# Kernel optimization log

Hardware: AMD Instinct MI355X
Metric: run time of the kernel (lower is better)

Reference implementation:

```python
import jax, jax.numpy as jnp
import numpy as np

DIM = 512
HEADS = 8
DIM_HEAD = 64
INNER = HEADS * DIM_HEAD          # 512
CPB_DIM = DIM // 2                # 256 (ContinuousPositionBias hidden dim)
FF_INNER = int(DIM * 4 * 2 / 3)   # 1365 (GEGLU inner dim)
B, C, F, H, W = 2, 512, 8, 32, 32
SCALE = DIM_HEAD ** -0.5


def setup_inputs() -> dict:
    key = jax.random.key(0)
    ks = jax.random.split(key, 24)
    def rnd(k, shape, s=0.02):
        return jax.random.normal(k, shape, jnp.float32) * s
    return {
        "x": jax.random.normal(ks[0], (B, C, F, W, W), jnp.float32)[:, :, :, :H, :],
        # spatial attention
        "sa_gamma": jnp.ones((DIM,), jnp.float32),
        "sa_wq": rnd(ks[1], (DIM, INNER)),
        "sa_wkv": rnd(ks[2], (DIM, 2 * INNER)),
        "sa_wo": rnd(ks[3], (INNER, DIM)),
        # temporal attention
        "ta_gamma": jnp.ones((DIM,), jnp.float32),
        "ta_wq": rnd(ks[4], (DIM, INNER)),
        "ta_wkv": rnd(ks[5], (DIM, 2 * INNER)),
        "ta_wo": rnd(ks[6], (INNER, DIM)),
        # spatial ContinuousPositionBias MLP (num_dims=2, layers=2)
        "sp_w1": rnd(ks[7], (2, CPB_DIM), 0.1), "sp_b1": jnp.zeros((CPB_DIM,), jnp.float32),
        "sp_w2": rnd(ks[8], (CPB_DIM, CPB_DIM), 0.05), "sp_b2": jnp.zeros((CPB_DIM,), jnp.float32),
        "sp_w3": rnd(ks[9], (CPB_DIM, HEADS), 0.05), "sp_b3": jnp.zeros((HEADS,), jnp.float32),
        # temporal ContinuousPositionBias MLP (num_dims=1)
        "tp_w1": rnd(ks[10], (1, CPB_DIM), 0.1), "tp_b1": jnp.zeros((CPB_DIM,), jnp.float32),
        "tp_w2": rnd(ks[11], (CPB_DIM, CPB_DIM), 0.05), "tp_b2": jnp.zeros((CPB_DIM,), jnp.float32),
        "tp_w3": rnd(ks[12], (CPB_DIM, HEADS), 0.05), "tp_b3": jnp.zeros((HEADS,), jnp.float32),
        # FeedForward: Conv3d 1x1 (no bias) -> GEGLU -> RMSNorm -> Conv3d 1x1
        "ff_win": rnd(ks[13], (DIM, 2 * FF_INNER)),
        "ff_gamma": jnp.ones((FF_INNER,), jnp.float32),
        "ff_wout": rnd(ks[14], (FF_INNER, DIM)),
    }


def _rms_last(x, g):
    # torch: F.normalize(x, dim=-1) * sqrt(C) * gamma
    nrm = jnp.sqrt(jnp.sum(x * x, axis=-1, keepdims=True))
    return x / jnp.maximum(nrm, 1e-12) * jnp.sqrt(jnp.float32(x.shape[-1])) * g


def _mlp_bias(rel, w1, b1, w2, b2, w3, b3):
    h = jax.nn.silu(rel @ w1 + b1)
    h = jax.nn.silu(h @ w2 + b2)
    return h @ w3 + b3  # [R, heads]


def _cpb_2d(h, w, params):
    ry = jnp.arange(-(h - 1), h, dtype=jnp.float32)
    rx = jnp.arange(-(w - 1), w, dtype=jnp.float32)
    gy, gx = jnp.meshgrid(ry, rx, indexing='ij')
    rel = jnp.stack([gy, gx], -1).reshape(-1, 2)          # [(2h-1)(2w-1), 2]
    tab = _mlp_bias(rel, *params)                          # [R, heads]
    py, px = jnp.meshgrid(jnp.arange(h), jnp.arange(w), indexing='ij')
    pos = jnp.stack([py.reshape(-1), px.reshape(-1)], -1)  # [n, 2]
    d = pos[:, None, :] - pos[None, :, :]                  # [n, n, 2]
    idx = (d[..., 0] + h - 1) * (2 * w - 1) + (d[..., 1] + w - 1)
    return jnp.transpose(tab[idx], (2, 0, 1))              # [heads, n, n]


def _cpb_1d(f, params):
    rel = jnp.arange(-(f - 1), f, dtype=jnp.float32)[:, None]
    tab = _mlp_bias(rel, *params)                          # [2f-1, heads]
    p = jnp.arange(f)
    idx = p[:, None] - p[None, :] + f - 1
    return jnp.transpose(tab[idx], (2, 0, 1))              # [heads, f, f]


def _attn(x, gamma, wq, wkv, wo, bias):
    # x: [b, n, c]; manual softmax(QK^T*scale + bias)V (flash disabled by pos_bias)
    xn = _rms_last(x, gamma)
    q = xn @ wq
    k, v = jnp.split(xn @ wkv, 2, axis=-1)
    b, n, _ = q.shape
    rs = lambda t: t.reshape(b, n, HEADS, DIM_HEAD).transpose(0, 2, 1, 3)
    q, k, v = rs(q), rs(k), rs(v)
    s = jnp.einsum('bhid,bhjd->bhij', q, k) * SCALE + bias[None]
    a = jax.nn.softmax(s, axis=-1)
    o = jnp.einsum('bhij,bhjd->bhid', a, v)
    o = o.transpose(0, 2, 1, 3).reshape(b, n, INNER)
    return o @ wo


def _ff(x, win, gamma, wout):
    # x: [b, f, h, w, c] channel-last; Conv3d 1x1 == channel einsum
    hdn = jnp.einsum('bfhwc,co->bfhwo', x, win)
    a, gate = jnp.split(hdn, 2, axis=-1)
    y = a * jax.nn.gelu(gate, approximate=False)           # GEGLU (torch exact gelu)
    # shift_token: chunk channels, shift second half by +1 frame
    c1 = (FF_INNER + 1) // 2
    t1, t2 = y[..., :c1], y[..., c1:]
    t2 = jnp.pad(t2, ((0, 0), (1, 0), (0, 0), (0, 0), (0, 0)))[:, :-1]
    y = jnp.concatenate([t1, t2], axis=-1)
    yn = _rms_last(y, gamma)                               # RMSNorm over channels
    return jnp.einsum('bfhwi,ic->bfhwc', yn, wout)


def reference(x, sa_gamma, sa_wq, sa_wkv, sa_wo, ta_gamma, ta_wq, ta_wkv, ta_wo,
              sp_w1, sp_b1, sp_w2, sp_b2, sp_w3, sp_b3,
              tp_w1, tp_b1, tp_w2, tp_b2, tp_w3, tp_b3,
              ff_win, ff_gamma, ff_wout):
    b, c, f, h, w = x.shape
    xl = jnp.transpose(x, (0, 2, 3, 4, 1))                 # b f h w c
    # spatial attention over (h w) tokens, batched over (b f)
    xs = xl.reshape(b * f, h * w, c)
    sp_bias = _cpb_2d(h, w, (sp_w1, sp_b1, sp_w2, sp_b2, sp_w3, sp_b3))
    xs = _attn(xs, sa_gamma, sa_wq, sa_wkv, sa_wo, sp_bias) + xs
    xv = xs.reshape(b, f, h, w, c)
    # temporal attention over f tokens, batched over (b h w)
    xt = jnp.transpose(xv, (0, 2, 3, 1, 4)).reshape(b * h * w, f, c)
    tp_bias = _cpb_1d(f, (tp_w1, tp_b1, tp_w2, tp_b2, tp_w3, tp_b3))
    xt = _attn(xt, ta_gamma, ta_wq, ta_wkv, ta_wo, tp_bias) + xt
    xv = jnp.transpose(xt.reshape(b, h, w, f, c), (0, 3, 1, 2, 4))
    # GEGLU feedforward with token shift
    xv = _ff(xv, ff_win, ff_gamma, ff_wout) + xv
    return jnp.transpose(xv, (0, 4, 1, 2, 3))              # b c f h w
```

## Files before the change

kernel.cpp:

```cpp
#include <hip/hip_runtime.h>
#include <cstdint>
#include <cstddef>

typedef __bf16 bf16_t;
typedef __bf16 bf16x8 __attribute__((ext_vector_type(8)));
typedef __bf16 bf16x4 __attribute__((ext_vector_type(4)));
typedef float floatx4 __attribute__((ext_vector_type(4)));

__device__ __forceinline__ float wred_sum(float v) {
#pragma unroll
  for (int off = 32; off > 0; off >>= 1) v += __shfl_xor(v, off);
  return v;
}
__device__ __forceinline__ void async16(const void* g, void* l) {
  __builtin_amdgcn_global_load_lds((const __attribute__((address_space(1))) void*)g,
                                   (__attribute__((address_space(3))) void*)l, 16, 0, 0);
}

template <int MODE>
__global__ __launch_bounds__(256) void st_gemm(
    const bf16_t* __restrict__ A, const bf16_t* __restrict__ B, void* Cp, void* Cp2,
    const float* Res, int M, int N, int K, int lda, int ldb, int ldc) {
  __shared__ bf16_t sA[3][128 * 32];
  __shared__ bf16_t sB[3][128 * 32];
  const int tid = threadIdx.x;
  const int bm = blockIdx.x, bn = blockIdx.y;
  const int lane = tid & 63;
  const int wave = tid >> 6;
  const int wm = (wave >> 1) * 64, wn = (wave & 1) * 64;
  const int rowf = lane & 15, qc = lane >> 4;
  const int fco = (qc ^ ((rowf >> 1) & 3)) * 8;

  const bf16_t* aSrc[2];
  const bf16_t* bSrc[2];
  int sOff[2];
#pragma unroll
  for (int it = 0; it < 2; ++it) {
    int slot = it * 256 + tid;
    int mi = slot >> 2, kc = slot & 3;
    int cs = kc ^ ((mi >> 1) & 3);
    int ar = bm * 128 + mi; if (ar > M - 1) ar = M - 1;
    int br = bn * 128 + mi; if (br > N - 1) br = N - 1;
    aSrc[it] = A + (size_t)ar * lda + cs * 8;
    bSrc[it] = B + (size_t)br * ldb + cs * 8;
    sOff[it] = slot * 16;
  }

  floatx4 acc[4][4];
#pragma unroll
  for (int i = 0; i < 4; ++i)
#pragma unroll
    for (int j = 0; j < 4; ++j) acc[i][j] = floatx4{0.f, 0.f, 0.f, 0.f};

  const int NT = K >> 5;
#pragma unroll
  for (int it = 0; it < 2; ++it) {
    async16(aSrc[it], (char*)sA[0] + sOff[it]);
    async16(bSrc[it], (char*)sB[0] + sOff[it]);
  }
#pragma unroll
  for (int it = 0; it < 2; ++it) {
    async16(aSrc[it] + 32, (char*)sA[1] + sOff[it]);
    async16(bSrc[it] + 32, (char*)sB[1] + sOff[it]);
  }
  __builtin_amdgcn_sched_barrier(0);
  asm volatile("s_waitcnt vmcnt(4)" ::: "memory");
  __builtin_amdgcn_s_barrier();
  __builtin_amdgcn_sched_barrier(0);

  int bcur = 0, bnx = 2;
#pragma unroll 1
  for (int t = 0; t < NT; ++t) {
    const bf16_t* sAc = sA[bcur];
    const bf16_t* sBc = sB[bcur];
    bf16x8 af[4], bv[4];
#pragma unroll
    for (int i = 0; i < 4; ++i) {
      af[i] = *(const bf16x8*)(sAc + (wm + i * 16 + rowf) * 32 + fco);
      bv[i] = *(const bf16x8*)(sBc + (wn + i * 16 + rowf) * 32 + fco);
    }
    if (t + 2 < NT) {
      const int kt2 = (t + 2) * 32;
#pragma unroll
      for (int it = 0; it < 2; ++it) {
        async16(aSrc[it] + kt2, (char*)sA[bnx] + sOff[it]);
        async16(bSrc[it] + kt2, (char*)sB[bnx] + sOff[it]);
      }
    }
#pragma unroll
    for (int i = 0; i < 4; ++i)
#pragma unroll
      for (int j = 0; j < 4; ++j)
        acc[i][j] = __builtin_amdgcn_mfma_f32_16x16x32_bf16(af[i], bv[j], acc[i][j], 0, 0, 0);
    if (t + 1 < NT) {
      __builtin_amdgcn_sched_barrier(0);
      if (t + 2 < NT) asm volatile("s_waitcnt vmcnt(4)" ::: "memory");
      else            asm volatile("s_waitcnt vmcnt(0)" ::: "memory");
      __builtin_amdgcn_s_barrier();
      __builtin_amdgcn_sched_barrier(0);
    }
    bcur = (bcur == 2) ? 0 : bcur + 1;
    bnx = (bnx == 2) ? 0 : bnx + 1;
  }

  const int cl = lane & 15;
  const int rowBase = bm * 128 + wm + (lane >> 4) * 4;
  if (MODE == 5) {
    bf16_t* yb = (bf16_t*)Cp;
    const int cg0 = ((bn * 128 + wn) >> 5) * 16;
#pragma unroll
    for (int i = 0; i < 4; ++i) {
#pragma unroll
      for (int p = 0; p < 2; ++p) {
        int c = cg0 + p * 16 + cl;
        if (c >= 1365) continue;
#pragma unroll
        for (int r = 0; r < 4; ++r) {
          int row = rowBase + i * 16 + r;
          if (row >= M) continue;
          float a = acc[i][2 * p][r];
          float gt = acc[i][2 * p + 1][r];
          float zz = gt * (0.7978845608f + 0.03567740814f * gt * gt);
          float u = __builtin_exp2f(-2.8853900817779268f * zz);
          float y = a * gt / (1.f + u);
          yb[(size_t)row * ldc + c] = (bf16_t)y;
        }
      }
    }
    return;
  }
  const int colBase = bn * 128 + wn + cl;
#pragma unroll
  for (int i = 0; i < 4; ++i) {
#pragma unroll
    for (int j = 0; j < 4; ++j) {
      int col = colBase + j * 16;
      if (col >= N) continue;
#pragma unroll
      for (int r = 0; r < 4; ++r) {
        int row = rowBase + i * 16 + r;
        if (row >= M) continue;
        long long inidx = (long long)row * ldc + col;
        float v = acc[i][j][r];
        if (MODE >= 2) v += Res[inidx];
        if (MODE == 1) { ((bf16_t*)Cp)[inidx] = (bf16_t)v; }
        else if (MODE == 2) { ((float*)Cp)[inidx] = v; }
        else if (MODE == 3) {
          int orow = (row & ~8191) | ((row & 1023) << 3) | ((row >> 10) & 7);
          ((float*)Cp)[(long long)orow * ldc + col] = v;
        } else if (MODE == 4) {
          int orow = (row & ~8191) | ((row & 7) << 10) | ((row >> 3) & 1023);
          long long oidx = (long long)orow * ldc + col;
          ((float*)Cp)[oidx] = v;
          ((bf16_t*)Cp2)[oidx] = (bf16_t)v;
        }
      }
    }
  }
}

__global__ __launch_bounds__(256) void st_transpose2d(
    const float* __restrict__ in, float* __restrict__ out, int R, int Cc,
    long long inb, long long outb) {
  __shared__ float tile[32][33];
  const int ct = blockIdx.x, rt = blockIdx.y, b = blockIdx.z;
  in += (long long)b * inb;
  out += (long long)b * outb;
  const int tx = threadIdx.x & 31, ty = threadIdx.x >> 5;
#pragma unroll
  for (int k = 0; k < 4; ++k) {
    int r = rt * 32 + ty + k * 8;
    int c = ct * 32 + tx;
    tile[ty + k * 8][tx] = in[(size_t)r * Cc + c];
  }
  __syncthreads();
#pragma unroll
  for (int k = 0; k < 4; ++k) {
    int c = ct * 32 + ty + k * 8;
    int r = rt * 32 + tx;
    out[(size_t)c * R + r] = tile[tx][ty + k * 8];
  }
}

__global__ void st_wtrans(const float* __restrict__ src, bf16_t* __restrict__ dst,
                          int K, int Kpad, int N, int srcld, int coloff, long total) {
  long idx = (long)blockIdx.x * 256 + threadIdx.x;
  if (idx >= total) return;
  int kp = (int)(idx % Kpad);
  int n = (int)(idx / Kpad);
  float v = (kp < K) ? src[(size_t)kp * srcld + coloff + n] : 0.f;
  dst[idx] = (bf16_t)v;
}

__global__ void st_wtrans_geglu(const float* __restrict__ src, bf16_t* __restrict__ dst,
                                long total) {
  long idx = (long)blockIdx.x * 256 + threadIdx.x;
  if (idx >= total) return;
  int kp = (int)(idx & 511);
  int n = (int)(idx >> 9);
  int c = ((n >> 5) << 4) + (n & 15);
  float v = 0.f;
  if (c < 1365) {
    int srccol = c + (((n >> 4) & 1) ? 1365 : 0);
    v = src[(size_t)kp * 2730 + srccol];
  }
  dst[idx] = (bf16_t)v;
}

__global__ __launch_bounds__(256) void st_cpb(
    const float* __restrict__ w1, const float* __restrict__ b1,
    const float* __restrict__ w2, const float* __restrict__ b2,
    const float* __restrict__ w3, const float* __restrict__ b3,
    float* __restrict__ tab2d, float* __restrict__ tab1d, int two_d) {
  const int pos = blockIdx.x, t = threadIdx.x;
  float r0, r1 = 0.f;
  if (two_d) { r0 = (float)(pos / 63 - 31); r1 = (float)(pos % 63 - 31); }
  else { r0 = (float)(pos - 7); }
  __shared__ float sh[256];
  float h = r0 * w1[t] + (two_d ? r1 * w1[256 + t] : 0.f) + b1[t];
  h = h / (1.f + expf(-h));
  sh[t] = h;
  __syncthreads();
  float h2 = b2[t];
  for (int j = 0; j < 256; ++j) h2 += sh[j] * w2[j * 256 + t];
  h2 = h2 / (1.f + expf(-h2));
  __syncthreads();
  sh[t] = h2;
  __syncthreads();
  if (t < 8) {
    float o = b3[t];
    for (int j = 0; j < 256; ++j) o += sh[j] * w3[j * 8 + t];
    if (two_d) tab2d[t * 4000 + pos] = o * 8.0f;
    else tab1d[t * 15 + pos] = o;
  }
}

__global__ __launch_bounds__(256) void st_rmsnorm(const float* __restrict__ x,
                                                  const float* __restrict__ gamma,
                                                  bf16_t* __restrict__ y) {
  const int token = blockIdx.x * 4 + (threadIdx.x >> 6);
  const int lane = threadIdx.x & 63;
  const float* xr = x + (size_t)token * 512;
  float v[8];
  float ss = 0.f;
#pragma unroll
  for (int k = 0; k < 8; ++k) { v[k] = xr[k * 64 + lane]; ss += v[k] * v[k]; }
  ss = wred_sum(ss);
  const float r = 22.627416998f / fmaxf(sqrtf(ss), 1e-12f);
  bf16_t* yr = y + (size_t)token * 512;
#pragma unroll
  for (int k = 0; k < 8; ++k) yr[k * 64 + lane] = (bf16_t)(v[k] * r * gamma[k * 64 + lane]);
}

__global__ __launch_bounds__(256) void st_vtrans(const bf16_t* __restrict__ qkv,
                                                 bf16_t* __restrict__ vT) {
  __shared__ float tile[32][33];
  const int jt = blockIdx.x, dt = blockIdx.y, z = blockIdx.z;
  const int bf = z >> 3, h = z & 7;
  const int tx = threadIdx.x & 31, ty = threadIdx.x >> 5;
#pragma unroll
  for (int k = 0; k < 4; ++k) {
    int j = jt * 32 + ty + k * 8;
    int d = dt * 32 + tx;
    tile[ty + k * 8][tx] = (float)qkv[((size_t)(bf * 1024 + j)) * 1536 + 1024 + h * 64 + d];
  }
  __syncthreads();
#pragma unroll
  for (int k = 0; k < 4; ++k) {
    int d = dt * 32 + ty + k * 8;
    int j = jt * 32 + tx;
    vT[((size_t)z * 64 + d) * 1024 + j] = (bf16_t)tile[tx][ty + k * 8];
  }
}

__global__ __launch_bounds__(256, 4) void st_flash(
    const bf16_t* __restrict__ qkv, const bf16_t* __restrict__ vT,
    const float* __restrict__ tab2f, bf16_t* __restrict__ ob) {
  __shared__ __align__(16) bf16_t ldsK[2][32 * 64];
  __shared__ __align__(16) bf16_t ldsV[2][64 * 32];
  __shared__ __align__(16) bf16_t ldsP[4 * 32 * 32];
  __shared__ __align__(16) float ldsT[2208];
  const int qtile = blockIdx.x;
  const int z = blockIdx.y;
  const int bf = z >> 3, h = z & 7;
  const int tid = threadIdx.x;
  const int lane = tid & 63, wave = tid >> 6;
  const int cl = lane & 15, g = lane >> 4;
  const size_t qkvBase = (size_t)bf * 1024 * 1536 + h * 64;
  const int eoff = (qtile * 252) & ~3;
  const bf16_t* Kp = qkv + qkvBase + 512;
  const bf16_t* Vp = vT + (size_t)z * 65536;

#pragma unroll
  for (int it = 0; it < 3; ++it) {
    int s = it * 256 + tid;
    if (s < 552) async16(tab2f + h * 4000 + eoff + s * 4, (char*)ldsT + s * 16);
  }
  {
    int row = tid >> 3, c = tid & 7, cs = c ^ (row & 7);
    async16(Kp + (size_t)row * 1536 + cs * 8, (char*)ldsK[0] + tid * 16);
    int rv = tid >> 2, cv = tid & 3, csv = cv ^ (rv & 3);
    async16(Vp + (size_t)rv * 1024 + csv * 8, (char*)ldsV[0] + tid * 16);
  }
  bf16x8 aq[2][2];
#pragma unroll
  for (int it = 0; it < 2; ++it)
#pragma unroll
    for (int ks = 0; ks < 2; ++ks) {
      int row = qtile * 128 + wave * 32 + it * 16 + cl;
      aq[it][ks] = *(const bf16x8*)(qkv + qkvBase + (size_t)row * 1536 + (ks * 4 + g) * 8);
    }
  __syncthreads();

  int fiB[2];
#pragma unroll
  for (int it = 0; it < 2; ++it) {
    int i = qtile * 128 + wave * 32 + it * 16 + cl;
    fiB[it] = (i >> 5) * 63 + (i & 31) + 1984 - eoff;
  }
  float lsum[2] = {0.f, 0.f};
  floatx4 oacc[4][2];
#pragma unroll
  for (int dt = 0; dt < 4; ++dt)
#pragma unroll
    for (int it = 0; it < 2; ++it) oacc[dt][it] = floatx4{0.f, 0.f, 0.f, 0.f};

  bf16_t* ldsPw = ldsP + wave * (32 * 32);
  const float SC = 0.18033688011112042f;

#pragma unroll 2
  for (int t = 0; t < 32; ++t) {
    const int p = t & 1;
    if (t < 31) {
      const int j1 = (t + 1) * 32;
      int row = tid >> 3, c = tid & 7, cs = c ^ (row & 7);
      async16(Kp + (size_t)(j1 + row) * 1536 + cs * 8, (char*)ldsK[p ^ 1] + tid * 16);
      int rv = tid >> 2, cv = tid & 3, csv = cv ^ (rv & 3);
      async16(Vp + (size_t)rv * 1024 + j1 + csv * 8, (char*)ldsV[p ^ 1] + tid * 16);
    }
    const int j0 = t * 32;
#pragma unroll
    for (int jt = 0; jt < 2; ++jt) {
      int jb = j0 + jt * 16 + g * 4;
      int fjb = (jb >> 5) * 63 + (jb & 31);
      floatx4 sj[2];
#pragma unroll
      for (int it = 0; it < 2; ++it) {
        int idx0 = fiB[it] - fjb;
        sj[it] = floatx4{ldsT[idx0], ldsT[idx0 - 1], ldsT[idx0 - 2], ldsT[idx0 - 3]};
      }
#pragma unroll
      for (int ks = 0; ks < 2; ++ks) {
        int row = jt * 16 + cl;
        bf16x8 kf = *(const bf16x8*)(ldsK[p] + row * 64 + (((ks * 4 + g) ^ (row & 7))) * 8);
#pragma unroll
        for (int it = 0; it < 2; ++it)
          sj[it] = __builtin_amdgcn_mfma_f32_16x16x32_bf16(kf, aq[it][ks], sj[it], 0, 0, 0);
      }
      int gg = jt * 2 + (g >> 1);
#pragma unroll
      for (int it = 0; it < 2; ++it) {
        float e0 = __builtin_exp2f(sj[it][0] * SC);
        float e1 = __builtin_exp2f(sj[it][1] * SC);
        float e2 = __builtin_exp2f(sj[it][2] * SC);
        float e3 = __builtin_exp2f(sj[it][3] * SC);
        lsum[it] += (e0 + e1) + (e2 + e3);
        bf16x4 pv = {(bf16_t)e0, (bf16_t)e1, (bf16_t)e2, (bf16_t)e3};
        *(bf16x4*)((char*)ldsPw + (it * 16 + cl) * 64 +
                   ((gg ^ (cl & 3)) * 16 + (g & 1) * 8)) = pv;
      }
    }
    {
      bf16x8 pB[2];
#pragma unroll
      for (int it = 0; it < 2; ++it)
        pB[it] = *(const bf16x8*)((char*)ldsPw + (it * 16 + cl) * 64 + ((g ^ (cl & 3)) * 16));
#pragma unroll
      for (int dt = 0; dt < 4; ++dt) {
        int row = dt * 16 + cl;
        bf16x8 vf = *(const bf16x8*)(ldsV[p] + row * 32 + ((g ^ (row & 3)) * 8));
#pragma unroll
        for (int it = 0; it < 2; ++it)
          oacc[dt][it] = __builtin_amdgcn_mfma_f32_16x16x32_bf16(vf, pB[it], oacc[dt][it], 0, 0, 0);
      }
    }
    __syncthreads();
  }
  float inv[2];
#pragma unroll
  for (int it = 0; it < 2; ++it) {
    float s = lsum[it];
    s += __shfl_xor(s, 16);
    s += __shfl_xor(s, 32);
    inv[it] = 1.f / s;
  }
#pragma unroll
  for (int it = 0; it < 2; ++it) {
    int i = qtile * 128 + wave * 32 + it * 16 + cl;
    size_t base = ((size_t)bf * 1024 + i) * 512 + h * 64 + g * 4;
#pragma unroll
    for (int dt = 0; dt < 4; ++dt) {
      bf16x4 ov = {(bf16_t)(oacc[dt][it][0] * inv[it]), (bf16_t)(oacc[dt][it][1] * inv[it]),
                   (bf16_t)(oacc[dt][it][2] * inv[it]), (bf16_t)(oacc[dt][it][3] * inv[it])};
      *(bf16x4*)(ob + base + dt * 16) = ov;
    }
  }
}

__global__ __launch_bounds__(256) void st_tattn2(const bf16_t* __restrict__ qkv,
                                                 const float* __restrict__ tabf,
                                                 bf16_t* __restrict__ o) {
  const int wg = blockIdx.x * 4 + (threadIdx.x >> 6);
  const int bhw = wg >> 3, head = wg & 7;
  const int lane = threadIdx.x & 63;
  const size_t base = (size_t)bhw * 8 * 1536 + head * 64 + lane;
  float q[8], k[8], v[8];
#pragma unroll
  for (int f = 0; f < 8; ++f) {
    q[f] = (float)qkv[base + (size_t)f * 1536];
    k[f] = (float)qkv[base + (size_t)f * 1536 + 512];
    v[f] = (float)qkv[base + (size_t)f * 1536 + 1024];
  }
  float p[64];
#pragma unroll
  for (int i = 0; i < 8; ++i)
#pragma unroll
    for (int j = 0; j < 8; ++j) p[i * 8 + j] = q[i] * k[j];
#pragma unroll
  for (int st = 32; st >= 1; st >>= 1) {
    const bool hi = (lane & st) != 0;
#pragma unroll
    for (int m = 0; m < st; ++m) {
      float give = hi ? p[m] : p[m + st];
      float keep = hi ? p[m + st] : p[m];
      p[m] = keep + __shfl_xor(give, st);
    }
  }
  const int i = lane >> 3, j = lane & 7;
  float e = __expf(p[0] * 0.125f + tabf[head * 15 + i - j + 7]);
  float sm = e;
  sm += __shfl_xor(sm, 1);
  sm += __shfl_xor(sm, 2);
  sm += __shfl_xor(sm, 4);
  const float prob = e / sm;
  float acc[8];
#pragma unroll
  for (int ii = 0; ii < 8; ++ii) acc[ii] = 0.f;
#pragma unroll
  for (int ii = 0; ii < 8; ++ii)
#pragma unroll
    for (int jj = 0; jj < 8; ++jj)
      acc[ii] += __shfl(prob, ii * 8 + jj) * v[jj];
#pragma unroll
  for (int ii = 0; ii < 8; ++ii)
    o[(size_t)(bhw * 8 + ii) * 512 + head * 64 + lane] = (bf16_t)acc[ii];
}

__global__ __launch_bounds__(256) void st_glu(const bf16_t* __restrict__ y,
                                              const float* __restrict__ gamma,
                                              bf16_t* __restrict__ yn) {
  const int t = blockIdx.x;
  const int tid = threadIdx.x;
  const int f = (t >> 10) & 7;
  float yv[6];
  float ss = 0.f;
#pragma unroll
  for (int kk = 0; kk < 6; ++kk) {
    int c = kk * 256 + tid;
    float v = 0.f;
    if (c < 1365) {
      long src = t;
      bool valid = true;
      if (c >= 683) { if (f == 0) valid = false; else src = t - 1024; }
      if (valid) v = (float)y[src * 1365 + c];
    }
    yv[kk] = v;
    ss += v * v;
  }
  __shared__ float red[4];
  ss = wred_sum(ss);
  if ((tid & 63) == 0) red[tid >> 6] = ss;
  __syncthreads();
  ss = red[0] + red[1] + red[2] + red[3];
  const float r = sqrtf(1365.f) / fmaxf(sqrtf(ss), 1e-12f);
#pragma unroll
  for (int kk = 0; kk < 6; ++kk) {
    int c = kk * 256 + tid;
    if (c < 1365) yn[(size_t)t * 1376 + c] = (bf16_t)(yv[kk] * r * gamma[c]);
  }
  if (tid < 11) yn[(size_t)t * 1376 + 1365 + tid] = (bf16_t)0.f;
}

extern "C" void kernel_launch(void* const* d_in, const int* in_sizes, int n_in,
                              void* d_out, int out_size, void* d_ws, size_t ws_size,
                              hipStream_t stream) {
  const float* x        = (const float*)d_in[0];
  const float* sa_gamma = (const float*)d_in[1];
  const float* sa_wq    = (const float*)d_in[2];
  const float* sa_wkv   = (const float*)d_in[3];
  const float* sa_wo    = (const float*)d_in[4];
  const float* ta_gamma = (const float*)d_in[5];
  const float* ta_wq    = (const float*)d_in[6];
  const float* ta_wkv   = (const float*)d_in[7];
  const float* ta_wo    = (const float*)d_in[8];
  const float* sp_w1 = (const float*)d_in[9];
  const float* sp_b1 = (const float*)d_in[10];
  const float* sp_w2 = (const float*)d_in[11];
  const float* sp_b2 = (const float*)d_in[12];
  const float* sp_w3 = (const float*)d_in[13];
  const float* sp_b3 = (const float*)d_in[14];
  const float* tp_w1 = (const float*)d_in[15];
  const float* tp_b1 = (const float*)d_in[16];
  const float* tp_w2 = (const float*)d_in[17];
  const float* tp_b2 = (const float*)d_in[18];
  const float* tp_w3 = (const float*)d_in[19];
  const float* tp_b3 = (const float*)d_in[20];
  const float* ff_win   = (const float*)d_in[21];
  const float* ff_gamma = (const float*)d_in[22];
  const float* ff_wout  = (const float*)d_in[23];
  float* outp = (float*)d_out;

  char* ws = (char*)d_ws;
  size_t off = 0;
  auto alloc = [&](size_t bytes) -> char* {
    char* p = ws + off;
    off += (bytes + 255) & ~(size_t)255;
    return p;
  };
  const long T = 16384;
  float*  xs  = (float*)alloc((size_t)T * 512 * 4);
  bf16_t* xn  = (bf16_t*)alloc((size_t)T * 512 * 2);
  char*   R2  = alloc((size_t)T * 1536 * 2);
  char*   R3  = alloc((size_t)T * 1536 * 2);
  char*   R4  = alloc((size_t)T * 1376 * 2);
  bf16_t* wqkvT_sa = (bf16_t*)alloc(1536ULL * 512 * 2);
  bf16_t* woT_sa   = (bf16_t*)alloc(512ULL * 512 * 2);
  bf16_t* wqkvT_ta = (bf16_t*)alloc(1536ULL * 512 * 2);
  bf16_t* woT_ta   = (bf16_t*)alloc(512ULL * 512 * 2);
  bf16_t* winT  = (bf16_t*)alloc(2752ULL * 512 * 2);
  bf16_t* woutT = (bf16_t*)alloc(512ULL * 1376 * 2);
  float*  tab2f = (float*)alloc(8 * 4000 * 4);
  float*  tabf  = (float*)alloc(8 * 15 * 4);

  bf16_t* qkv  = (bf16_t*)R2;
  bf16_t* ybuf = (bf16_t*)R2;
  bf16_t* vT   = (bf16_t*)R3;
  float*  xt   = (float*)R3;
  bf16_t* ob_s = xn;
  bf16_t* ob_t = (bf16_t*)R4;
  bf16_t* ynb  = (bf16_t*)R4;

  st_transpose2d<<<dim3(256, 16, 2), 256, 0, stream>>>(x, xs, 512, 8192,
                                                       (long long)512 * 8192, (long long)512 * 8192);
  auto wt = [&](const float* src, bf16_t* dst, int K, int Kpad, int N, int srcld, int coloff) {
    long tot = (long)N * Kpad;
    st_wtrans<<<dim3((tot + 255) / 256), 256, 0, stream>>>(src, dst, K, Kpad, N, srcld, coloff, tot);
  };
  wt(sa_wq, wqkvT_sa, 512, 512, 512, 512, 0);
  wt(sa_wkv, wqkvT_sa + 512 * 512, 512, 512, 1024, 1024, 0);
  wt(sa_wo, woT_sa, 512, 512, 512, 512, 0);
  wt(ta_wq, wqkvT_ta, 512, 512, 512, 512, 0);
  wt(ta_wkv, wqkvT_ta + 512 * 512, 512, 512, 1024, 1024, 0);
  wt(ta_wo, woT_ta, 512, 512, 512, 512, 0);
  st_wtrans_geglu<<<dim3((2752 * 512) / 256), 256, 0, stream>>>(ff_win, winT, 2752L * 512);
  wt(ff_wout, woutT, 1365, 1376, 512, 512, 0);
  st_cpb<<<dim3(3969), 256, 0, stream>>>(sp_w1, sp_b1, sp_w2, sp_b2, sp_w3, sp_b3, tab2f, tabf, 1);
  st_cpb<<<dim3(15), 256, 0, stream>>>(tp_w1, tp_b1, tp_w2, tp_b2, tp_w3, tp_b3, tab2f, tabf, 0);

  st_rmsnorm<<<dim3(4096), 256, 0, stream>>>(xs, sa_gamma, xn);
  st_gemm<1><<<dim3(128, 12), 256, 0, stream>>>(
      xn, wqkvT_sa, (void*)qkv, nullptr, nullptr, 16384, 1536, 512, 512, 512, 1536);
  st_vtrans<<<dim3(32, 2, 128), 256, 0, stream>>>(qkv, vT);
  st_flash<<<dim3(8, 128), 256, 0, stream>>>(qkv, vT, tab2f, ob_s);
  st_gemm<3><<<dim3(128, 4), 256, 0, stream>>>(
      ob_s, woT_sa, (void*)xt, nullptr, xs, 16384, 512, 512, 512, 512, 512);

  st_rmsnorm<<<dim3(4096), 256, 0, stream>>>(xt, ta_gamma, xn);
  st_gemm<1><<<dim3(128, 12), 256, 0, stream>>>(
      xn, wqkvT_ta, (void*)qkv, nullptr, nullptr, 16384, 1536, 512, 512, 512, 1536);
  st_tattn2<<<dim3(4096), 256, 0, stream>>>(qkv, tabf, ob_t);
  st_gemm<4><<<dim3(128, 4), 256, 0, stream>>>(
      ob_t, woT_ta, (void*)xs, (void*)xn, xt, 16384, 512, 512, 512, 512, 512);

  st_gemm<5><<<dim3(128, 22), 256, 0, stream>>>(
      xn, winT, (void*)ybuf, nullptr, nullptr, 16384, 2752, 512, 512, 512, 1365);
  st_glu<<<dim3(16384), 256, 0, stream>>>(ybuf, ff_gamma, ynb);
  st_gemm<2><<<dim3(128, 4), 256, 0, stream>>>(
      ynb, woutT, (void*)xs, nullptr, xs, 16384, 512, 1376, 1376, 1376, 512);

  st_transpose2d<<<dim3(16, 256, 2), 256, 0, stream>>>(xs, outp, 8192, 512,
                                                       (long long)8192 * 512, (long long)8192 * 512);
}
```

Baseline: 654.9 us.

## Triple-buffer K in flash attention, read V directly from global, swap grid order

The spatial flash-attention kernel now keeps K in a three-stage LDS ring with prefetch two tiles ahead. The barrier is replaced by an explicit vmcnt wait plus s_barrier, so only one global load is in flight per wait. V fragments are read straight from global memory (the transposed vT buffer), dropping the V LDS staging. The P scratch uses a padded row stride of 80 bytes instead of an XOR swizzle. The grid is swapped so consecutive blocks share a qtile across heads, which changes the L2 access pattern. Direct global V reads add latency inside the loop, and the hand-tuned waitcnt makes correctness depend on async load ordering.

Result: no change. 658.0 us (+0.5%).

```diff
diff --git a/kernel.cpp b/kernel.cpp
--- a/kernel.cpp
+++ b/kernel.cpp
@@ -276,12 +276,11 @@
 __global__ __launch_bounds__(256, 4) void st_flash(
     const bf16_t* __restrict__ qkv, const bf16_t* __restrict__ vT,
     const float* __restrict__ tab2f, bf16_t* __restrict__ ob) {
-  __shared__ __align__(16) bf16_t ldsK[2][32 * 64];
-  __shared__ __align__(16) bf16_t ldsV[2][64 * 32];
-  __shared__ __align__(16) bf16_t ldsP[4 * 32 * 32];
+  __shared__ __align__(16) bf16_t ldsK[3][32 * 64];
+  __shared__ __align__(16) char ldsP[4 * 32 * 80];
   __shared__ __align__(16) float ldsT[2208];
-  const int qtile = blockIdx.x;
-  const int z = blockIdx.y;
+  const int z = blockIdx.x;
+  const int qtile = blockIdx.y;
   const int bf = z >> 3, h = z & 7;
   const int tid = threadIdx.x;
   const int lane = tid & 63, wave = tid >> 6;
@@ -296,12 +295,10 @@
     int s = it * 256 + tid;
     if (s < 552) async16(tab2f + h * 4000 + eoff + s * 4, (char*)ldsT + s * 16);
   }
-  {
-    int row = tid >> 3, c = tid & 7, cs = c ^ (row & 7);
-    async16(Kp + (size_t)row * 1536 + cs * 8, (char*)ldsK[0] + tid * 16);
-    int rv = tid >> 2, cv = tid & 3, csv = cv ^ (rv & 3);
-    async16(Vp + (size_t)rv * 1024 + csv * 8, (char*)ldsV[0] + tid * 16);
-  }
+  const int krow = tid >> 3, kc = tid & 7;
+  const bf16_t* kSrc = Kp + (size_t)krow * 1536 + (kc ^ (krow & 7)) * 8;
+  async16(kSrc, (char*)ldsK[0] + tid * 16);
+  async16(kSrc + (size_t)32 * 1536, (char*)ldsK[1] + tid * 16);
   bf16x8 aq[2][2];
 #pragma unroll
   for (int it = 0; it < 2; ++it)
@@ -310,6 +307,9 @@
       int row = qtile * 128 + wave * 32 + it * 16 + cl;
       aq[it][ks] = *(const bf16x8*)(qkv + qkvBase + (size_t)row * 1536 + (ks * 4 + g) * 8);
     }
+  const bf16_t* vPtr[4];
+#pragma unroll
+  for (int dt = 0; dt < 4; ++dt) vPtr[dt] = Vp + (size_t)(dt * 16 + cl) * 1024 + g * 8;
   __syncthreads();
 
   int fiB[2];
@@ -325,19 +325,13 @@
 #pragma unroll
     for (int it = 0; it < 2; ++it) oacc[dt][it] = floatx4{0.f, 0.f, 0.f, 0.f};
 
-  bf16_t* ldsPw = ldsP + wave * (32 * 32);
+  char* ldsPw = ldsP + wave * 2560;
   const float SC = 0.18033688011112042f;
 
-#pragma unroll 2
+  int bcur = 0, bnx = 2;
+#pragma unroll 1
   for (int t = 0; t < 32; ++t) {
-    const int p = t & 1;
-    if (t < 31) {
-      const int j1 = (t + 1) * 32;
-      int row = tid >> 3, c = tid & 7, cs = c ^ (row & 7);
-      async16(Kp + (size_t)(j1 + row) * 1536 + cs * 8, (char*)ldsK[p ^ 1] + tid * 16);
-      int rv = tid >> 2, cv = tid & 3, csv = cv ^ (rv & 3);
-      async16(Vp + (size_t)rv * 1024 + j1 + csv * 8, (char*)ldsV[p ^ 1] + tid * 16);
-    }
+    const bf16_t* Kc = ldsK[bcur];
     const int j0 = t * 32;
 #pragma unroll
     for (int jt = 0; jt < 2; ++jt) {
@@ -352,12 +346,11 @@
 #pragma unroll
       for (int ks = 0; ks < 2; ++ks) {
         int row = jt * 16 + cl;
-        bf16x8 kf = *(const bf16x8*)(ldsK[p] + row * 64 + (((ks * 4 + g) ^ (row & 7))) * 8);
+        bf16x8 kf = *(const bf16x8*)(Kc + row * 64 + (((ks * 4 + g) ^ (row & 7))) * 8);
 #pragma unroll
         for (int it = 0; it < 2; ++it)
           sj[it] = __builtin_amdgcn_mfma_f32_16x16x32_bf16(kf, aq[it][ks], sj[it], 0, 0, 0);
       }
-      int gg = jt * 2 + (g >> 1);
 #pragma unroll
       for (int it = 0; it < 2; ++it) {
         float e0 = __builtin_exp2f(sj[it][0] * SC);
@@ -366,25 +359,32 @@
         float e3 = __builtin_exp2f(sj[it][3] * SC);
         lsum[it] += (e0 + e1) + (e2 + e3);
         bf16x4 pv = {(bf16_t)e0, (bf16_t)e1, (bf16_t)e2, (bf16_t)e3};
-        *(bf16x4*)((char*)ldsPw + (it * 16 + cl) * 64 +
-                   ((gg ^ (cl & 3)) * 16 + (g & 1) * 8)) = pv;
+        *(bf16x4*)(ldsPw + (it * 16 + cl) * 80 + (jt * 4 + g) * 8) = pv;
       }
     }
     {
       bf16x8 pB[2];
 #pragma unroll
       for (int it = 0; it < 2; ++it)
-        pB[it] = *(const bf16x8*)((char*)ldsPw + (it * 16 + cl) * 64 + ((g ^ (cl & 3)) * 16));
+        pB[it] = *(const bf16x8*)(ldsPw + (it * 16 + cl) * 80 + g * 16);
 #pragma unroll
       for (int dt = 0; dt < 4; ++dt) {
-        int row = dt * 16 + cl;
-        bf16x8 vf = *(const bf16x8*)(ldsV[p] + row * 32 + ((g ^ (row & 3)) * 8));
+        bf16x8 vf = *(const bf16x8*)(vPtr[dt] + j0);
 #pragma unroll
         for (int it = 0; it < 2; ++it)
           oacc[dt][it] = __builtin_amdgcn_mfma_f32_16x16x32_bf16(vf, pB[it], oacc[dt][it], 0, 0, 0);
       }
     }
-    __syncthreads();
+    if (t + 2 < 32) async16(kSrc + (size_t)(t + 2) * 32 * 1536, (char*)ldsK[bnx] + tid * 16);
+    if (t + 1 < 32) {
+      __builtin_amdgcn_sched_barrier(0);
+      if (t + 2 < 32) asm volatile("s_waitcnt vmcnt(1)" ::: "memory");
+      else            asm volatile("s_waitcnt vmcnt(0)" ::: "memory");
+      __builtin_amdgcn_s_barrier();
+      __builtin_amdgcn_sched_barrier(0);
+    }
+    bcur = (bcur == 2) ? 0 : bcur + 1;
+    bnx = (bnx == 2) ? 0 : bnx + 1;
   }
   float inv[2];
 #pragma unroll
@@ -571,7 +571,7 @@
   st_gemm<1><<<dim3(128, 12), 256, 0, stream>>>(
       xn, wqkvT_sa, (void*)qkv, nullptr, nullptr, 16384, 1536, 512, 512, 512, 1536);
   st_vtrans<<<dim3(32, 2, 128), 256, 0, stream>>>(qkv, vT);
-  st_flash<<<dim3(8, 128), 256, 0, stream>>>(qkv, vT, tab2f, ob_s);
+  st_flash<<<dim3(128, 8), 256, 0, stream>>>(qkv, vT, tab2f, ob_s);
   st_gemm<3><<<dim3(128, 4), 256, 0, stream>>>(
       ob_s, woT_sa, (void*)xt, nullptr, xs, 16384, 512, 512, 512, 512, 512);
 
```
